# Performance work log

Measured on AMD Instinct MI355X. Metric: run time of the kernel, lower is better.

## Reference

```python
import jax, jax.numpy as jnp
import numpy as np

VOCAB, EMBED, HIDDEN, NCLS, PAD = 50257, 512, 1024, 2, 0

def setup_inputs() -> dict:
    key = jax.random.key(0)
    ks = jax.random.split(key, 16)
    def xavier(k, shape):
        fan_in, fan_out = shape[1], shape[0]
        lim = jnp.sqrt(6.0 / (fan_in + fan_out))
        return jax.random.uniform(k, shape, jnp.float32, -lim, lim)
    x = jax.random.randint(ks[0], (64, 512), 0, VOCAB, dtype=jnp.int32)
    emb = jax.random.uniform(ks[1], (VOCAB, EMBED), jnp.float32, -0.1, 0.1)
    emb = emb.at[PAD].set(0.0)
    return {
        'x': x,
        'emb': emb,
        'W_ii': xavier(ks[2], (HIDDEN, EMBED)), 'b_ii': jnp.zeros((HIDDEN,), jnp.float32),
        'W_hi': xavier(ks[3], (HIDDEN, HIDDEN)),
        'W_if': xavier(ks[4], (HIDDEN, EMBED)), 'b_if': jnp.zeros((HIDDEN,), jnp.float32),
        'W_hf': xavier(ks[5], (HIDDEN, HIDDEN)),
        'W_ig': xavier(ks[6], (HIDDEN, EMBED)), 'b_ig': jnp.zeros((HIDDEN,), jnp.float32),
        'W_hg': xavier(ks[7], (HIDDEN, HIDDEN)),
        'W_io': xavier(ks[8], (HIDDEN, EMBED)), 'b_io': jnp.zeros((HIDDEN,), jnp.float32),
        'W_ho': xavier(ks[9], (HIDDEN, HIDDEN)),
        'V_w': xavier(ks[10], (NCLS, HIDDEN)), 'V_b': jnp.zeros((NCLS,), jnp.float32),
    }


def _lstm_forward(x, emb, W_ii, b_ii, W_hi, W_if, b_if, W_hf, W_ig, b_ig, W_hg, W_io, b_io, W_ho, V_w, V_b):
    # Dropout layers act as identity in eval mode.
    e = emb[x]  # [B,S,E]
    B, S, E = e.shape
    H = W_hi.shape[0]
    # Precompute all input-to-gate projections in one batched GEMM.
    Wx = jnp.stack([W_ii, W_if, W_ig, W_io], axis=0)      # [4,H,E]
    bx = jnp.stack([b_ii, b_if, b_ig, b_io], axis=0)      # [4,H]
    gates_x = jnp.einsum('bse,ghe->sbgh', e, Wx) + bx     # [S,B,4,H]
    Wh = jnp.stack([W_hi, W_hf, W_hg, W_ho], axis=0)      # [4,H,H]

    def step(carry, gx):
        h, c = carry
        gh = jnp.einsum('bk,ghk->bgh', h, Wh)             # [B,4,H]
        g = gx + gh
        i_t = jax.nn.sigmoid(g[:, 0])
        f_t = jax.nn.sigmoid(g[:, 1])
        g_t = jnp.tanh(g[:, 2])
        o_t = jax.nn.sigmoid(g[:, 3])
        c = f_t * c + i_t * g_t
        h = o_t * jnp.tanh(c)
        return (h, c), None

    h0 = jnp.zeros((B, H), e.dtype)
    c0 = jnp.zeros((B, H), e.dtype)
    (h, c), _ = jax.lax.scan(step, (h0, c0), gates_x)
    out = h @ V_w.T + V_b
    return out, (h, c)


def reference(x, emb, W_ii, b_ii, W_hi, W_if, b_if, W_hf, W_ig, b_ig, W_hg, W_io, b_io, W_ho, V_w, V_b):
    return _lstm_forward(x, emb, W_ii, b_ii, W_hi, W_if, b_if, W_hf, W_ig, b_ig, W_hg, W_io, b_io, W_ho, V_w, V_b)
```

## Files before the change

### kernel.cpp

```cpp
#include <hip/hip_runtime.h>
#include <math.h>

#define Bn 64
#define Hn 1024
#define En 512
#define Sn 512
#define RING 32

typedef _Float16 f16;
typedef _Float16 half8 __attribute__((ext_vector_type(8)));
typedef float f32x4 __attribute__((ext_vector_type(4)));


__global__ __launch_bounds__(256) void wpack_kernel(
    const float* __restrict__ Whi_, const float* __restrict__ Whf_,
    const float* __restrict__ Whg_, const float* __restrict__ Who_,
    const float* __restrict__ Wxi_, const float* __restrict__ Wxf_,
    const float* __restrict__ Wxg_, const float* __restrict__ Wxo_,
    f16* __restrict__ wpHi, f16* __restrict__ wpLo)
{
    int t = blockIdx.x * 256 + threadIdx.x;
    int lane = t & 63;
    int rest = t >> 6;
    int kc = rest % 48;
    int bb = rest / 48;
    int n = lane & 15, g = n >> 2, du = n & 3;
    int u = bb * 4 + du;
    int klo = (lane >> 4) << 3;
    const float* Wh = (g == 0 ? Whi_ : g == 1 ? Whf_ : g == 2 ? Whg_ : Who_);
    const float* Wx = (g == 0 ? Wxi_ : g == 1 ? Wxf_ : g == 2 ? Wxg_ : Wxo_);
    const float* src = (kc < 32) ? (Wh + (size_t)u * Hn + kc * 32 + klo)
                                 : (Wx + (size_t)u * En + (kc - 32) * 32 + klo);
    float4 v0 = ((const float4*)src)[0];
    float4 v1 = ((const float4*)src)[1];
    float w[8] = {v0.x, v0.y, v0.z, v0.w, v1.x, v1.y, v1.z, v1.w};
    #pragma unroll
    for (int j = 0; j < 8; ++j) {
        f16 hi = (f16)w[j];
        float lo = (w[j] - (float)hi) * 2048.0f;
        wpHi[(size_t)t * 8 + j] = hi;
        wpLo[(size_t)t * 8 + j] = (f16)lo;
    }
}

__global__ __launch_bounds__(256) void epack_kernel(
    const int* __restrict__ x, const float* __restrict__ emb,
    f16* __restrict__ eF)
{
    int t = blockIdx.x * 256 + threadIdx.x;
    int lane = t & 63;
    int q = t >> 6;
    int mt = q & 3; q >>= 2;
    int kc2 = q & 15;
    int s = q >> 4;
    int b = mt * 16 + (lane & 15);
    int tok = x[b * Sn + s];
    int k = kc2 * 32 + ((lane >> 4) << 3);
    const float* src = emb + (size_t)tok * En + k;
    float4 v0 = ((const float4*)src)[0];
    float4 v1 = ((const float4*)src)[1];
    f16* dst = eF + (size_t)t * 8;
    dst[0] = (f16)v0.x; dst[1] = (f16)v0.y; dst[2] = (f16)v0.z; dst[3] = (f16)v0.w;
    dst[4] = (f16)v1.x; dst[5] = (f16)v1.y; dst[6] = (f16)v1.z; dst[7] = (f16)v1.w;
}

__global__ __launch_bounds__(256) void gx_chunk_kernel(
    const half8* __restrict__ eF,
    const half8* __restrict__ wpHi, const half8* __restrict__ wpLo,
    float* __restrict__ gx, int chunk)
{
    int lane = threadIdx.x & 63;
    int id = blockIdx.x * 4 + (threadIdx.x >> 6);
    int sc = id >> 8;
    int bb = id & 255;
    int s = chunk * RING + sc;

    const half8* eFs = eF + (size_t)s * 4096 + lane;
    const half8* bH = wpHi + ((size_t)(bb * 48 + 32)) * 64 + lane;
    const half8* bL = wpLo + ((size_t)(bb * 48 + 32)) * 64 + lane;

    f32x4 aH[4], aL[4];
    #pragma unroll
    for (int mt = 0; mt < 4; ++mt) { aH[mt] = (f32x4)0.0f; aL[mt] = (f32x4)0.0f; }

    for (int kcx = 0; kcx < 16; ++kcx) {
        half8 bh = bH[(size_t)kcx * 64];
        half8 bl = bL[(size_t)kcx * 64];
        #pragma unroll
        for (int mt = 0; mt < 4; ++mt) {
            half8 a = eFs[(size_t)((kcx * 4 + mt) * 64)];
            aH[mt] = __builtin_amdgcn_mfma_f32_16x16x32_f16(a, bh, aH[mt], 0, 0, 0);
            aL[mt] = __builtin_amdgcn_mfma_f32_16x16x32_f16(a, bl, aL[mt], 0, 0, 0);
        }
    }

    int n = lane & 15, g = n >> 2, du = n & 3;
    int col = (g << 10) + bb * 4 + du;
    float* g0 = gx + (size_t)sc * (Bn * 4096) + col;
    #pragma unroll
    for (int mt = 0; mt < 4; ++mt) {
        #pragma unroll
        for (int r = 0; r < 4; ++r) {
            int b = mt * 16 + ((lane >> 4) << 2) + r;
            g0[(size_t)b * 4096] = aH[mt][r] + aL[mt][r] * (1.0f / 2048.0f);
        }
    }
}

template<bool USE_GX>
__global__ __launch_bounds__(1024) void step_kernel(
    const f16* __restrict__ hFin, f16* __restrict__ hFout,
    const half8* __restrict__ eF,
    const half8* __restrict__ wpHi, const half8* __restrict__ wpLo,
    const float* __restrict__ gx,
    const float* __restrict__ bi, const float* __restrict__ bf,
    const float* __restrict__ bg, const float* __restrict__ bo,
    float* __restrict__ c, float* __restrict__ hFinal, int s)
{
    __shared__ float preW[16][256];

    const int tid  = threadIdx.x;
    const int lane = tid & 63;
    const int wv   = tid >> 6;
    const int mt   = wv & 3;
    const int kq   = wv >> 2;
    const int bb   = blockIdx.x;

    const half8* hin = (const half8*)hFin + lane;
    const half8* bHb = wpHi + (size_t)(bb * 48) * 64 + lane;
    const half8* bLb = wpLo + (size_t)(bb * 48) * 64 + lane;

    f32x4 accH = {0.f, 0.f, 0.f, 0.f};
    f32x4 accL = {0.f, 0.f, 0.f, 0.f};

    if (USE_GX) {
        #pragma unroll
        for (int i = 0; i < 8; ++i) {
            int kc = kq * 8 + i;
            half8 a  = hin[(size_t)((kc * 4 + mt) * 64)];
            half8 bh = bHb[(size_t)kc * 64];
            half8 bl = bLb[(size_t)kc * 64];
            accH = __builtin_amdgcn_mfma_f32_16x16x32_f16(a, bh, accH, 0, 0, 0);
            accL = __builtin_amdgcn_mfma_f32_16x16x32_f16(a, bl, accL, 0, 0, 0);
        }
    } else {
        const half8* eFs = eF + (size_t)s * 4096 + lane;
        #pragma unroll
        for (int i = 0; i < 12; ++i) {
            int kc = kq * 12 + i;
            half8 a = (kc < 32) ? hin[(size_t)((kc * 4 + mt) * 64)]
                                : eFs[(size_t)(((kc - 32) * 4 + mt) * 64)];
            half8 bh = bHb[(size_t)kc * 64];
            half8 bl = bLb[(size_t)kc * 64];
            accH = __builtin_amdgcn_mfma_f32_16x16x32_f16(a, bh, accH, 0, 0, 0);
            accL = __builtin_amdgcn_mfma_f32_16x16x32_f16(a, bl, accL, 0, 0, 0);
        }
    }

    f32x4 v;
    #pragma unroll
    for (int r = 0; r < 4; ++r) v[r] = accH[r] + accL[r] * (1.0f / 2048.0f);
    *(f32x4*)&preW[wv][lane * 4] = v;
    __syncthreads();

    if (tid < 256) {
        const int bcell = tid >> 2, ducell = tid & 3;
        const int colcell = bb * 4 + ducell;
        const int msub = bcell & 15, mtp = bcell >> 4;
        const int base_i = ((msub >> 2) * 16) * 4 + (msub & 3);
        float sg_[4];
        #pragma unroll
        for (int g = 0; g < 4; ++g) {
            int idx = base_i + (g * 4 + ducell) * 4;
            sg_[g] = preW[0 * 4 + mtp][idx] + preW[1 * 4 + mtp][idx]
                   + preW[2 * 4 + mtp][idx] + preW[3 * 4 + mtp][idx];
        }
        float si = sg_[0] + bi[colcell];
        float sf = sg_[1] + bf[colcell];
        float sg = sg_[2] + bg[colcell];
        float so = sg_[3] + bo[colcell];
        if (USE_GX) {
            const float* gr = gx + ((size_t)(s & (RING - 1)) * Bn + bcell) * 4096;
            si += gr[colcell];        sf += gr[1024 + colcell];
            sg += gr[2048 + colcell]; so += gr[3072 + colcell];
        }
        float it = 1.f / (1.f + expf(-si));
        float ft = 1.f / (1.f + expf(-sf));
        float gt = tanhf(sg);
        float ot = 1.f / (1.f + expf(-so));
        int gi = bcell * Hn + colcell;
        float cn = ft * c[gi] + it * gt;
        c[gi] = cn;
        float hn = ot * tanhf(cn);
        int kch = colcell >> 5, dk = colcell & 31;
        int lp  = ((dk >> 3) << 4) | (bcell & 15);
        int mtp2 = bcell >> 4;
        hFout[((size_t)((kch * 4 + mtp2) * 64 + lp)) * 8 + (dk & 7)] = (f16)hn;
        if (s == Sn - 1) hFinal[gi] = hn;
    }
}

__global__ __launch_bounds__(256) void copy_hc(
    const float* __restrict__ h, const float* __restrict__ c,
    float* __restrict__ out)
{
    int i = blockIdx.x * 256 + threadIdx.x;
    out[128 + i] = h[i];
    out[128 + Bn * Hn + i] = c[i];
}

__global__ __launch_bounds__(64) void classifier(
    const float* __restrict__ h, const float* __restrict__ Vw,
    const float* __restrict__ Vb, float* __restrict__ out)
{
    int bid = blockIdx.x;
    int b = bid >> 1, n = bid & 1;
    int lane = threadIdx.x;
    float sum = 0.f;
    for (int k = lane; k < Hn; k += 64)
        sum += h[b * Hn + k] * Vw[n * Hn + k];
    #pragma unroll
    for (int off = 32; off > 0; off >>= 1)
        sum += __shfl_down(sum, off, 64);
    if (lane == 0)
        out[b * 2 + n] = sum + Vb[n];
}


#define KT 128
#define KTP 132

__global__ __launch_bounds__(256) void lstm_step_fb(
    const int* __restrict__ x, const float* __restrict__ emb,
    const float* __restrict__ Wxi, const float* __restrict__ Wxf,
    const float* __restrict__ Wxg, const float* __restrict__ Wxo,
    const float* __restrict__ bi, const float* __restrict__ bf,
    const float* __restrict__ bg, const float* __restrict__ bo,
    const float* __restrict__ Whi, const float* __restrict__ Whf,
    const float* __restrict__ Whg, const float* __restrict__ Who,
    const float* __restrict__ h_in, const float* __restrict__ c_in,
    float* __restrict__ h_out, float* __restrict__ c_out, int s)
{
    __shared__ float sh[Bn][KTP];
    __shared__ float sw[16][KTP];
    const int tid = threadIdx.x;
    const int b = tid >> 2, j = tid & 3;
    const int cb = blockIdx.x * 4, col = cb + j;
    float acc0 = 0.f, acc1 = 0.f, acc2 = 0.f, acc3 = 0.f;

    for (int k0 = 0; k0 < En; k0 += KT) {
        for (int i = tid; i < Bn * (KT / 4); i += 256) {
            int bl = i >> 5, k4 = (i & 31) << 2;
            int tok = x[bl * Sn + s];
            *reinterpret_cast<float4*>(&sh[bl][k4]) =
                *reinterpret_cast<const float4*>(&emb[(size_t)tok * En + k0 + k4]);
        }
        for (int i = tid; i < 16 * (KT / 4); i += 256) {
            int r = i >> 5, k4 = (i & 31) << 2;
            const float* Wg = (r < 8) ? ((r < 4) ? Wxi : Wxf)
                                      : ((r < 12) ? Wxg : Wxo);
            *reinterpret_cast<float4*>(&sw[r][k4]) =
                *reinterpret_cast<const float4*>(&Wg[(size_t)(cb + (r & 3)) * En + k0 + k4]);
        }
        __syncthreads();
        #pragma unroll 8
        for (int k = 0; k < KT; k += 4) {
            float4 hv = *reinterpret_cast<const float4*>(&sh[b][k]);
            float4 w0 = *reinterpret_cast<const float4*>(&sw[j][k]);
            float4 w1 = *reinterpret_cast<const float4*>(&sw[4 + j][k]);
            float4 w2 = *reinterpret_cast<const float4*>(&sw[8 + j][k]);
            float4 w3 = *reinterpret_cast<const float4*>(&sw[12 + j][k]);
            acc0 += hv.x*w0.x + hv.y*w0.y + hv.z*w0.z + hv.w*w0.w;
            acc1 += hv.x*w1.x + hv.y*w1.y + hv.z*w1.z + hv.w*w1.w;
            acc2 += hv.x*w2.x + hv.y*w2.y + hv.z*w2.z + hv.w*w2.w;
            acc3 += hv.x*w3.x + hv.y*w3.y + hv.z*w3.z + hv.w*w3.w;
        }
        __syncthreads();
    }
    for (int k0 = 0; k0 < Hn; k0 += KT) {
        for (int i = tid; i < Bn * (KT / 4); i += 256) {
            int bl = i >> 5, k4 = (i & 31) << 2;
            *reinterpret_cast<float4*>(&sh[bl][k4]) =
                *reinterpret_cast<const float4*>(&h_in[(size_t)bl * Hn + k0 + k4]);
        }
        for (int i = tid; i < 16 * (KT / 4); i += 256) {
            int r = i >> 5, k4 = (i & 31) << 2;
            const float* Wg = (r < 8) ? ((r < 4) ? Whi : Whf)
                                      : ((r < 12) ? Whg : Who);
            *reinterpret_cast<float4*>(&sw[r][k4]) =
                *reinterpret_cast<const float4*>(&Wg[(size_t)(cb + (r & 3)) * Hn + k0 + k4]);
        }
        __syncthreads();
        #pragma unroll 8
        for (int k = 0; k < KT; k += 4) {
            float4 hv = *reinterpret_cast<const float4*>(&sh[b][k]);
            float4 w0 = *reinterpret_cast<const float4*>(&sw[j][k]);
            float4 w1 = *reinterpret_cast<const float4*>(&sw[4 + j][k]);
            float4 w2 = *reinterpret_cast<const float4*>(&sw[8 + j][k]);
            float4 w3 = *reinterpret_cast<const float4*>(&sw[12 + j][k]);
            acc0 += hv.x*w0.x + hv.y*w0.y + hv.z*w0.z + hv.w*w0.w;
            acc1 += hv.x*w1.x + hv.y*w1.y + hv.z*w1.z + hv.w*w1.w;
            acc2 += hv.x*w2.x + hv.y*w2.y + hv.z*w2.z + hv.w*w2.w;
            acc3 += hv.x*w3.x + hv.y*w3.y + hv.z*w3.z + hv.w*w3.w;
        }
        __syncthreads();
    }
    acc0 += bi[col]; acc1 += bf[col]; acc2 += bg[col]; acc3 += bo[col];
    float it = 1.f / (1.f + expf(-acc0));
    float ft = 1.f / (1.f + expf(-acc1));
    float gt = tanhf(acc2);
    float ot = 1.f / (1.f + expf(-acc3));
    float cn = ft * c_in[b * Hn + col] + it * gt;
    c_out[b * Hn + col] = cn;
    h_out[b * Hn + col] = ot * tanhf(cn);
}


extern "C" void kernel_launch(void* const* d_in, const int* in_sizes, int n_in,
                              void* d_out, int out_size, void* d_ws, size_t ws_size,
                              hipStream_t stream) {
    const int*   x   = (const int*)  d_in[0];
    const float* emb = (const float*)d_in[1];
    const float* Wxi = (const float*)d_in[2];
    const float* bi  = (const float*)d_in[3];
    const float* Whi = (const float*)d_in[4];
    const float* Wxf = (const float*)d_in[5];
    const float* bf  = (const float*)d_in[6];
    const float* Whf = (const float*)d_in[7];
    const float* Wxg = (const float*)d_in[8];
    const float* bg  = (const float*)d_in[9];
    const float* Whg = (const float*)d_in[10];
    const float* Wxo = (const float*)d_in[11];
    const float* bo  = (const float*)d_in[12];
    const float* Who = (const float*)d_in[13];
    const float* Vw  = (const float*)d_in[14];
    const float* Vb  = (const float*)d_in[15];
    float* out = (float*)d_out;

    const size_t szHF = (size_t)2 * 65536 * sizeof(f16);
    const size_t szC  = (size_t)Bn * Hn * sizeof(float);
    const size_t szEF = (size_t)Sn * 16 * 4 * 64 * 8 * sizeof(f16);
    const size_t szWp = (size_t)256 * 48 * 64 * 8 * sizeof(f16);
    const size_t szGx = (size_t)RING * Bn * 4096 * sizeof(float);
    const size_t need_mid = szHF + 2 * szC + szEF + 2 * szWp;
    const size_t need_gx  = need_mid + szGx;

    if (ws_size >= need_mid) {
        const bool useGx = (ws_size >= need_gx);
        char* base = (char*)d_ws;
        f16*   hF   = (f16*)base;   base += szHF;
        float* c    = (float*)base; base += szC;
        float* h    = (float*)base; base += szC;
        f16*   eF   = (f16*)base;   base += szEF;
        f16*   wpHi = (f16*)base;   base += szWp;
        f16*   wpLo = (f16*)base;   base += szWp;
        float* gx   = (float*)base;

        hipMemsetAsync(d_ws, 0, szHF + szC, stream);
        wpack_kernel<<<dim3(3072), dim3(256), 0, stream>>>(
            Whi, Whf, Whg, Who, Wxi, Wxf, Wxg, Wxo, wpHi, wpLo);
        epack_kernel<<<dim3(8192), dim3(256), 0, stream>>>(x, emb, eF);

        if (useGx) {
            for (int chunk = 0; chunk < Sn / RING; ++chunk) {
                gx_chunk_kernel<<<dim3(2048), dim3(256), 0, stream>>>(
                    (const half8*)eF, (const half8*)wpHi, (const half8*)wpLo,
                    gx, chunk);
                for (int sc = 0; sc < RING; ++sc) {
                    int s = chunk * RING + sc;
                    const f16* hin  = hF + (size_t)(s & 1) * 65536;
                    f16*       hout = hF + (size_t)((s + 1) & 1) * 65536;
                    step_kernel<true><<<dim3(256), dim3(1024), 0, stream>>>(
                        hin, hout, (const half8*)eF,
                        (const half8*)wpHi, (const half8*)wpLo,
                        gx, bi, bf, bg, bo, c, h, s);
                }
            }
        } else {
            for (int s = 0; s < Sn; ++s) {
                const f16* hin  = hF + (size_t)(s & 1) * 65536;
                f16*       hout = hF + (size_t)((s + 1) & 1) * 65536;
                step_kernel<false><<<dim3(256), dim3(1024), 0, stream>>>(
                    hin, hout, (const half8*)eF,
                    (const half8*)wpHi, (const half8*)wpLo,
                    (const float*)nullptr, bi, bf, bg, bo, c, h, s);
            }
        }
        copy_hc<<<dim3(Bn * Hn / 256), dim3(256), 0, stream>>>(h, c, out);
        classifier<<<dim3(Bn * 2), dim3(64), 0, stream>>>(h, Vw, Vb, out);
    } else {
        float* hA = (float*)d_ws;
        float* cA = hA + Bn * Hn;
        float* hB = cA + Bn * Hn;
        float* cB = hB + Bn * Hn;
        hipMemsetAsync(d_ws, 0, (size_t)2 * Bn * Hn * sizeof(float), stream);
        for (int s = 0; s < Sn; ++s) {
            const float* hi = (s & 1) ? hB : hA;
            const float* ci = (s & 1) ? cB : cA;
            float* ho = (s & 1) ? hA : hB;
            float* co = (s & 1) ? cA : cB;
            lstm_step_fb<<<dim3(Hn / 4), dim3(256), 0, stream>>>(
                x, emb, Wxi, Wxf, Wxg, Wxo, bi, bf, bg, bo,
                Whi, Whf, Whg, Who, hi, ci, ho, co, s);
        }
        copy_hc<<<dim3(Bn * Hn / 256), dim3(256), 0, stream>>>(hA, cA, out);
        classifier<<<dim3(Bn * 2), dim3(64), 0, stream>>>(hA, Vw, Vb, out);
    }
}
```

Before: 4.678 ms.

## Fuse per-chunk LSTM steps into a persistent cooperative kernel with grid barrier

```diff
diff --git a/kernel.cpp b/kernel.cpp
--- a/kernel.cpp
+++ b/kernel.cpp
@@ -6,6 +6,7 @@
 #define En 512
 #define Sn 512
 #define RING 32
+#define NBLK 256
 
 typedef _Float16 f16;
 typedef _Float16 half8 __attribute__((ext_vector_type(8)));
@@ -200,6 +201,164 @@
     }
 }
 
+__global__ __launch_bounds__(1024) void steps_chunk_coop(
+    f16* __restrict__ hF,
+    const half8* __restrict__ eF,
+    const half8* __restrict__ wpHi, const half8* __restrict__ wpLo,
+    float* __restrict__ gx,
+    const float* __restrict__ bi, const float* __restrict__ bf,
+    const float* __restrict__ bg, const float* __restrict__ bo,
+    float* __restrict__ c, float* __restrict__ hFinal,
+    unsigned* __restrict__ cnt, int chunk)
+{
+    __shared__ alignas(16) f16 wHs[32 * 512];
+    __shared__ alignas(16) f16 wLs[32 * 512];
+    __shared__ float preW[16][256];
+
+    const int tid  = threadIdx.x;
+    const int lane = tid & 63;
+    const int wv   = tid >> 6;
+    const int mt   = wv & 3;
+    const int kq   = wv >> 2;
+    const int bb   = blockIdx.x;
+
+    {
+        const half8* srcH = wpHi + (size_t)(bb * 48) * 64;
+        const half8* srcL = wpLo + (size_t)(bb * 48) * 64;
+        half8* dH = (half8*)wHs;
+        half8* dL = (half8*)wLs;
+        #pragma unroll
+        for (int i = 0; i < 2; ++i) {
+            dH[tid + i * 1024] = srcH[tid + i * 1024];
+            dL[tid + i * 1024] = srcL[tid + i * 1024];
+        }
+    }
+
+    {
+        const half8* bH = wpHi + ((size_t)(bb * 48 + 32)) * 64 + lane;
+        const half8* bL = wpLo + ((size_t)(bb * 48 + 32)) * 64 + lane;
+        #pragma unroll
+        for (int t2 = 0; t2 < 2; ++t2) {
+            int sc = wv * 2 + t2;
+            int s = chunk * RING + sc;
+            const half8* eFs = eF + (size_t)s * 4096 + lane;
+            f32x4 aH[4], aL[4];
+            #pragma unroll
+            for (int m2 = 0; m2 < 4; ++m2) { aH[m2] = (f32x4)0.0f; aL[m2] = (f32x4)0.0f; }
+            for (int kcx = 0; kcx < 16; ++kcx) {
+                half8 bh = bH[(size_t)kcx * 64];
+                half8 bl = bL[(size_t)kcx * 64];
+                #pragma unroll
+                for (int m2 = 0; m2 < 4; ++m2) {
+                    half8 a = eFs[(size_t)((kcx * 4 + m2) * 64)];
+                    aH[m2] = __builtin_amdgcn_mfma_f32_16x16x32_f16(a, bh, aH[m2], 0, 0, 0);
+                    aL[m2] = __builtin_amdgcn_mfma_f32_16x16x32_f16(a, bl, aL[m2], 0, 0, 0);
+                }
+            }
+            int n = lane & 15, g = n >> 2, du = n & 3;
+            int col = (g << 10) + bb * 4 + du;
+            float* g0 = gx + (size_t)sc * (Bn * 4096) + col;
+            #pragma unroll
+            for (int m2 = 0; m2 < 4; ++m2) {
+                #pragma unroll
+                for (int r = 0; r < 4; ++r) {
+                    int b = m2 * 16 + ((lane >> 4) << 2) + r;
+                    g0[(size_t)b * 4096] = aH[m2][r] + aL[m2][r] * (1.0f / 2048.0f);
+                }
+            }
+        }
+    }
+
+    float creg = 0.f, bi_r = 0.f, bf_r = 0.f, bg_r = 0.f, bo_r = 0.f;
+    int bcell = 0, ducell = 0, colcell = 0, gi = 0, mtp = 0, base_i = 0;
+    int kch = 0, dk = 0, lp = 0;
+    if (tid < 256) {
+        bcell = tid >> 2; ducell = tid & 3;
+        colcell = bb * 4 + ducell;
+        gi = bcell * Hn + colcell;
+        int msub = bcell & 15; mtp = bcell >> 4;
+        base_i = ((msub >> 2) * 16) * 4 + (msub & 3);
+        creg = c[gi];
+        bi_r = bi[colcell]; bf_r = bf[colcell];
+        bg_r = bg[colcell]; bo_r = bo[colcell];
+        kch = colcell >> 5; dk = colcell & 31;
+        lp  = ((dk >> 3) << 4) | (bcell & 15);
+    }
+
+    __syncthreads();
+
+    const half8* wHl = (const half8*)wHs + lane;
+    const half8* wLl = (const half8*)wLs + lane;
+
+    for (int sc = 0; sc < RING; ++sc) {
+        const int s = chunk * RING + sc;
+        const half8* hin = (const half8*)(hF + (size_t)(s & 1) * 65536) + lane;
+        f16* hout = hF + (size_t)((s + 1) & 1) * 65536;
+
+        float gxi = 0.f, gxf = 0.f, gxg = 0.f, gxo = 0.f;
+        if (tid < 256) {
+            const float* gr = gx + ((size_t)sc * Bn + bcell) * 4096;
+            gxi = gr[colcell];        gxf = gr[1024 + colcell];
+            gxg = gr[2048 + colcell]; gxo = gr[3072 + colcell];
+        }
+
+        f32x4 accH = {0.f, 0.f, 0.f, 0.f};
+        f32x4 accL = {0.f, 0.f, 0.f, 0.f};
+        #pragma unroll
+        for (int i = 0; i < 8; ++i) {
+            const int kc = kq * 8 + i;
+            half8 a  = hin[(size_t)((kc * 4 + mt) * 64)];
+            half8 bh = wHl[(size_t)kc * 64];
+            half8 bl = wLl[(size_t)kc * 64];
+            accH = __builtin_amdgcn_mfma_f32_16x16x32_f16(a, bh, accH, 0, 0, 0);
+            accL = __builtin_amdgcn_mfma_f32_16x16x32_f16(a, bl, accL, 0, 0, 0);
+        }
+        f32x4 v;
+        #pragma unroll
+        for (int r = 0; r < 4; ++r) v[r] = accH[r] + accL[r] * (1.0f / 2048.0f);
+        *(f32x4*)&preW[wv][lane * 4] = v;
+        __syncthreads();
+
+        if (tid < 256) {
+            float sg_[4];
+            #pragma unroll
+            for (int g = 0; g < 4; ++g) {
+                int idx = base_i + (g * 4 + ducell) * 4;
+                sg_[g] = preW[mtp][idx] + preW[4 + mtp][idx]
+                       + preW[8 + mtp][idx] + preW[12 + mtp][idx];
+            }
+            float si = sg_[0] + bi_r + gxi;
+            float sf = sg_[1] + bf_r + gxf;
+            float sg = sg_[2] + bg_r + gxg;
+            float so = sg_[3] + bo_r + gxo;
+            float it = 1.f / (1.f + expf(-si));
+            float ft = 1.f / (1.f + expf(-sf));
+            float gt = tanhf(sg);
+            float ot = 1.f / (1.f + expf(-so));
+            float cn = ft * creg + it * gt;
+            creg = cn;
+            float hn = ot * tanhf(cn);
+            hout[((size_t)((kch * 4 + mtp) * 64 + lp)) * 8 + (dk & 7)] = (f16)hn;
+            if (s == Sn - 1) hFinal[gi] = hn;
+        }
+
+        __syncthreads();
+        if (tid == 0) {
+            __threadfence();
+            __hip_atomic_fetch_add(cnt, 1u, __ATOMIC_RELEASE,
+                                   __HIP_MEMORY_SCOPE_AGENT);
+            const unsigned need = (unsigned)(chunk * RING + sc + 1) * NBLK;
+            while (__hip_atomic_load(cnt, __ATOMIC_RELAXED,
+                                     __HIP_MEMORY_SCOPE_AGENT) < need)
+                __builtin_amdgcn_s_sleep(1);
+            __threadfence();
+        }
+        __syncthreads();
+    }
+
+    if (tid < 256) c[gi] = creg;
+}
+
 __global__ __launch_bounds__(256) void copy_hc(
     const float* __restrict__ h, const float* __restrict__ c,
     float* __restrict__ out)
@@ -342,11 +501,13 @@
     const size_t szEF = (size_t)Sn * 16 * 4 * 64 * 8 * sizeof(f16);
     const size_t szWp = (size_t)256 * 48 * 64 * 8 * sizeof(f16);
     const size_t szGx = (size_t)RING * Bn * 4096 * sizeof(float);
-    const size_t need_mid = szHF + 2 * szC + szEF + 2 * szWp;
-    const size_t need_gx  = need_mid + szGx;
+    const size_t need_mid  = szHF + 2 * szC + szEF + 2 * szWp;
+    const size_t need_gx   = need_mid + szGx;
+    const size_t need_coop = need_gx + 4096;
 
     if (ws_size >= need_mid) {
-        const bool useGx = (ws_size >= need_gx);
+        const bool haveGx   = (ws_size >= need_gx);
+        const bool haveCoop = (ws_size >= need_coop);
         char* base = (char*)d_ws;
         f16*   hF   = (f16*)base;   base += szHF;
         float* c    = (float*)base; base += szC;
@@ -354,26 +515,50 @@
         f16*   eF   = (f16*)base;   base += szEF;
         f16*   wpHi = (f16*)base;   base += szWp;
         f16*   wpLo = (f16*)base;   base += szWp;
-        float* gx   = (float*)base;
+        float* gx   = (float*)base; base += szGx;
+        unsigned* cnt = (unsigned*)base;
 
         hipMemsetAsync(d_ws, 0, szHF + szC, stream);
+        if (haveCoop) hipMemsetAsync(cnt, 0, 128, stream);
         wpack_kernel<<<dim3(3072), dim3(256), 0, stream>>>(
             Whi, Whf, Whg, Who, Wxi, Wxf, Wxg, Wxo, wpHi, wpLo);
         epack_kernel<<<dim3(8192), dim3(256), 0, stream>>>(x, emb, eF);
 
-        if (useGx) {
+        if (haveGx) {
+            bool coop = haveCoop;
             for (int chunk = 0; chunk < Sn / RING; ++chunk) {
-                gx_chunk_kernel<<<dim3(2048), dim3(256), 0, stream>>>(
-                    (const half8*)eF, (const half8*)wpHi, (const half8*)wpLo,
-                    gx, chunk);
-                for (int sc = 0; sc < RING; ++sc) {
-                    int s = chunk * RING + sc;
-                    const f16* hin  = hF + (size_t)(s & 1) * 65536;
-                    f16*       hout = hF + (size_t)((s + 1) & 1) * 65536;
-                    step_kernel<true><<<dim3(256), dim3(1024), 0, stream>>>(
-                        hin, hout, (const half8*)eF,
-                        (const half8*)wpHi, (const half8*)wpLo,
-                        gx, bi, bf, bg, bo, c, h, s);
+                if (coop) {
+                    f16* hFp = hF;
+                    const half8* eF8   = (const half8*)eF;
+                    const half8* wpHi8 = (const half8*)wpHi;
+                    const half8* wpLo8 = (const half8*)wpLo;
+                    float* gxp = gx;
+                    const float* bip = bi; const float* bfp = bf;
+                    const float* bgp = bg; const float* bop = bo;
+                    float* cp = c; float* hp = h;
+                    unsigned* cntp = cnt;
+                    int ci = chunk;
+                    void* args[] = { &hFp, &eF8, &wpHi8, &wpLo8, &gxp,
+                                     &bip, &bfp, &bgp, &bop, &cp, &hp,
+                                     &cntp, &ci };
+                    hipError_t e = hipLaunchCooperativeKernel(
+                        (const void*)steps_chunk_coop, dim3(NBLK), dim3(1024),
+                        args, 0, stream);
+                    if (e != hipSuccess) { coop = false; (void)hipGetLastError(); }
+                }
+                if (!coop) {
+                    gx_chunk_kernel<<<dim3(2048), dim3(256), 0, stream>>>(
+                        (const half8*)eF, (const half8*)wpHi, (const half8*)wpLo,
+                        gx, chunk);
+                    for (int sc = 0; sc < RING; ++sc) {
+                        int s = chunk * RING + sc;
+                        const f16* hin  = hF + (size_t)(s & 1) * 65536;
+                        f16*       hout = hF + (size_t)((s + 1) & 1) * 65536;
+                        step_kernel<true><<<dim3(256), dim3(1024), 0, stream>>>(
+                            hin, hout, (const half8*)eF,
+                            (const half8*)wpHi, (const half8*)wpLo,
+                            gx, bi, bf, bg, bo, c, h, s);
+                    }
                 }
             }
         } else {
```

Measured after the change: 12.62 ms. +169.7%, slower.
